# Kernel tuning notes

Hardware: AMD Instinct MI355X
Metric: run time of the kernel (lower is better)

## Reference

```python
import jax, jax.numpy as jnp
import numpy as np
from jax import lax

BN_EPS = 1e-5


def _condconv(x, w, b, fc_w, fc_b):
    """CondConv2D: per-sample expert mixing then 3x3 conv (pad=1, stride=1).
    x: [B, Cin, H, W]; w: [E, Cout, Cin, 3, 3]; b: [Cout]; fc_w: [E, Cin]; fc_b: [E].
    """
    B, Cin, H, W = x.shape
    E, Cout, _, kh, kw = w.shape
    pooled = x.mean(axis=(2, 3))                               # [B, Cin] adaptive_avg_pool2d(1,1)+flatten
    rw = jax.nn.sigmoid(pooled @ fc_w.T + fc_b)                # [B, E] routing weights
    kernels = jnp.einsum('be,eoihw->boihw', rw, w)             # [B, Cout, Cin, 3, 3]
    # Batched per-sample conv via grouped conv: groups = B
    xi = x.reshape(1, B * Cin, H, W)
    ker = kernels.reshape(B * Cout, Cin, kh, kw)
    out = lax.conv_general_dilated(
        xi, ker, window_strides=(1, 1), padding=((1, 1), (1, 1)),
        feature_group_count=B,
        dimension_numbers=('NCHW', 'OIHW', 'NCHW'))
    return out.reshape(B, Cout, H, W) + b[None, :, None, None]


def _bn_relu(x, g, b, m, v):
    # eval-mode BatchNorm2d followed by ReLU
    inv = g * lax.rsqrt(v + BN_EPS)
    return jax.nn.relu(x * inv[None, :, None, None] + (b - m * inv)[None, :, None, None])


def setup_inputs() -> dict:
    key = jax.random.key(0)
    ks = jax.random.split(key, 8)
    B, Cin, Cout, H, W, E = 16, 64, 128, 128, 128, 3
    s1 = 1.0 / np.sqrt(Cin * 9)
    s2 = 1.0 / np.sqrt(Cout * 9)
    return {
        'x': jax.random.normal(ks[0], (B, Cin, H, W), jnp.float32),
        'w1': jax.random.normal(ks[1], (E, Cout, Cin, 3, 3), jnp.float32) * s1,
        'b1': jax.random.normal(ks[2], (Cout,), jnp.float32) * s1,
        'fc1_w': jax.random.normal(ks[3], (E, Cin), jnp.float32) / np.sqrt(Cin),
        'fc1_b': jnp.zeros((E,), jnp.float32),
        'bn1_g': jnp.ones((Cout,), jnp.float32),
        'bn1_b': jnp.zeros((Cout,), jnp.float32),
        'bn1_m': jnp.zeros((Cout,), jnp.float32),
        'bn1_v': jnp.ones((Cout,), jnp.float32),
        'w2': jax.random.normal(ks[4], (E, Cout, Cout, 3, 3), jnp.float32) * s2,
        'b2': jax.random.normal(ks[5], (Cout,), jnp.float32) * s2,
        'fc2_w': jax.random.normal(ks[6], (E, Cout), jnp.float32) / np.sqrt(Cout),
        'fc2_b': jnp.zeros((E,), jnp.float32),
        'bn2_g': jnp.ones((Cout,), jnp.float32),
        'bn2_b': jnp.zeros((Cout,), jnp.float32),
        'bn2_m': jnp.zeros((Cout,), jnp.float32),
        'bn2_v': jnp.ones((Cout,), jnp.float32),
    }


def reference(x, w1, b1, fc1_w, fc1_b, bn1_g, bn1_b, bn1_m, bn1_v,
              w2, b2, fc2_w, fc2_b, bn2_g, bn2_b, bn2_m, bn2_v):
    h = _condconv(x, w1, b1, fc1_w, fc1_b)
    h = _bn_relu(h, bn1_g, bn1_b, bn1_m, bn1_v)
    h = _condconv(h, w2, b2, fc2_w, fc2_b)
    h = _bn_relu(h, bn2_g, bn2_b, bn2_m, bn2_v)
    return h
```

## Files before the change

kernel.cpp:

```cpp
#include <hip/hip_runtime.h>
#include <math.h>

#define BN_EPS 1e-5f

typedef short bf16x8 __attribute__((ext_vector_type(8)));
typedef float f32x4 __attribute__((ext_vector_type(4)));
typedef float f32x16 __attribute__((ext_vector_type(16)));
typedef unsigned short ushort8v __attribute__((ext_vector_type(8)));
typedef unsigned int uint;
typedef unsigned short ushort;

__device__ inline ushort f2bf(float f) {
    uint u = __float_as_uint(f);
    uint r = u + 0x7FFFu + ((u >> 16) & 1u);
    return (ushort)(r >> 16);
}
__device__ inline float bf2f(ushort u) { return __uint_as_float(((uint)u) << 16); }

__global__ void scsh_kernel(const float* b1, const float* g1, const float* bb1,
                            const float* m1, const float* v1,
                            const float* b2, const float* g2, const float* bb2,
                            const float* m2, const float* v2,
                            float* scsh1, float* scsh2) {
    int t = threadIdx.x;
    if (t < 128) {
        float sc = g1[t] * rsqrtf(v1[t] + BN_EPS);
        scsh1[t] = sc;
        scsh1[128 + t] = (b1[t] - m1[t]) * sc + bb1[t];
    } else {
        int c = t - 128;
        float sc = g2[c] * rsqrtf(v2[c] + BN_EPS);
        scsh2[c] = sc;
        scsh2[128 + c] = (b2[c] - m2[c]) * sc + bb2[c];
    }
}

__global__ void xprep_kernel(const float* __restrict__ x, ushort* __restrict__ xT,
                             float* __restrict__ pooled1) {
    __shared__ float t[64][65];
    const int b = blockIdx.y;
    const int p0 = blockIdx.x * 64;
    const int tid = threadIdx.x;
#pragma unroll
    for (int it = 0; it < 16; ++it) {
        const int idx = it * 256 + tid;
        const int ci = idx >> 6, p = idx & 63;
        t[ci][p] = x[((size_t)b * 64 + ci) * 16384 + p0 + p];
    }
    __syncthreads();
    const int h = p0 >> 7;
#pragma unroll
    for (int it = 0; it < 2; ++it) {
        const int p = it * 32 + (tid >> 3);
        const int w = (p0 & 127) + p;
        const int c0 = (tid & 7) * 8;
        const int cc = c0 >> 4;
        ushort8v u;
#pragma unroll
        for (int j = 0; j < 8; ++j) u[j] = f2bf(t[c0 + j][p]);
        *(ushort8v*)&xT[(((size_t)(b * 128 + h) * 4 + cc) * 128 + w) * 16 + (c0 & 15)] = u;
    }
    if (tid < 64) {
        float s = 0.f;
#pragma unroll 8
        for (int p = 0; p < 64; ++p) s += t[tid][p];
        atomicAdd(&pooled1[b * 64 + tid], s);
    }
}

__global__ void pool2h_kernel(const ushort* __restrict__ hT, float* __restrict__ pooled2) {
    const int b = blockIdx.x, slab = blockIdx.y;
    const int tid = threadIdx.x;
    const int cc = tid >> 5, o = (tid >> 4) & 1, wb = tid & 15;
    float a[8] = {0.f, 0.f, 0.f, 0.f, 0.f, 0.f, 0.f, 0.f};
    for (int r = 0; r < 4; ++r) {
        const int h = slab * 4 + r;
        const ushort* base = hT + ((size_t)(b * 128 + h) * 8 + cc) * 2048 + o * 8;
#pragma unroll
        for (int k = 0; k < 8; ++k) {
            const ushort8v u = *(const ushort8v*)(base + (wb + k * 16) * 16);
#pragma unroll
            for (int j = 0; j < 8; ++j) a[j] += bf2f(u[j]);
        }
    }
    __shared__ float sp[16][8][17];
    const int grp0 = cc * 2 + o;
#pragma unroll
    for (int j = 0; j < 8; ++j) sp[grp0][j][wb] = a[j];
    __syncthreads();
    if (tid < 128) {
        const int grp = tid >> 3, j = tid & 7;
        float s = 0.f;
#pragma unroll
        for (int k = 0; k < 16; ++k) s += sp[grp][j][k];
        const int c = (grp >> 1) * 16 + (grp & 1) * 8 + j;
        atomicAdd(&pooled2[b * 128 + c], s);
    }
}

template <int CIN>
__global__ void mix_route_kernel(const float* __restrict__ w, const float* __restrict__ pooled,
                                 const float* __restrict__ fcw, const float* __restrict__ fcb,
                                 ushort* __restrict__ wmix) {
    constexpr int NCC = CIN / 16;
    __shared__ float rwl[48];
    const int tid = threadIdx.x;
    if (tid < 48) {
        const int bb = tid / 3, e = tid % 3;
        float d = 0.f;
        for (int c = 0; c < CIN; ++c) d += pooled[bb * CIN + c] * fcw[e * CIN + c];
        const float s = fcb[e] + d * (1.f / 16384.f);
        rwl[tid] = 1.f / (1.f + expf(-s));
    }
    __syncthreads();
    const int co = blockIdx.x;
    const int sw = (co >> 2) & 1;
    for (int b = 0; b < 16; ++b) {
        const float r0 = rwl[b * 3 + 0], r1 = rwl[b * 3 + 1], r2 = rwl[b * 3 + 2];
        for (int idx = tid; idx < CIN * 9; idx += 256) {
            const int ci = idx & (CIN - 1);
            const int tap = idx / CIN;
            const size_t off = ((size_t)co * CIN + ci) * 9 + tap;
            const float m = r0 * w[off]
                          + r1 * w[off + (size_t)128 * CIN * 9]
                          + r2 * w[off + (size_t)2 * 128 * CIN * 9];
            const int cc = ci >> 4, o = (ci >> 3) & 1, e = ci & 7;
            const size_t dst = (((size_t)(b * NCC + cc)) * 2304
                             + (tap * 128 + co) * 2 + (o ^ sw)) * 8 + e;
            wmix[dst] = f2bf(m);
        }
    }
}

template <int CIN, bool TO_BF16>
__global__ __launch_bounds__(512, 2)
void conv_mfma5_kernel(const ushort* __restrict__ xT, const ushort* __restrict__ wmix,
                       const float* __restrict__ scsh,
                       float* __restrict__ outf, ushort* __restrict__ outh) {
    constexpr int NCC = CIN / 16;
    constexpr int IBUF = 24960;
    constexpr int WOFF = 2 * IBUF;
    constexpr int WBUF = 36864;
    __shared__ __align__(16) char smem[123648];

    const int L = ((blockIdx.x & 7) << 6) | (blockIdx.x >> 3);
    const int b = L >> 5;
    const int rt = L & 31;

    const int tid = threadIdx.x;
    const int lane = tid & 63, wid = tid >> 6;
    const int wm = wid >> 2, wn = wid & 3;
    const int l31 = lane & 31, lhi = lane >> 5;

    f32x16 acc[2][4];
#pragma unroll
    for (int i = 0; i < 2; ++i)
#pragma unroll
        for (int j = 0; j < 4; ++j)
#pragma unroll
            for (int r = 0; r < 16; ++r) acc[i][j][r] = 0.f;

    const ushort* inb = xT + (size_t)b * 128 * NCC * 2048;
    const ushort* wmb = wmix + (size_t)b * NCC * 18432;

    auto stage = [&](int bufi, int cc) {
        const ushort* wsrc = wmb + (size_t)cc * 18432;
        for (int j = wid; j < 60; j += 8) {
            if (j < 24) {
                const int r = j >> 2, i = j & 3;
                const int hg = rt * 4 - 1 + r;
                if ((unsigned)hg < 128u) {
                    const int q = i * 64 + lane;
                    const int cm1 = q >> 1;
                    const int so = (q & 1) ^ (((cm1 + 1) >> 2) & 1);
                    const ushort* src = inb + ((size_t)(hg * NCC + cc)) * 2048 + cm1 * 16 + so * 8;
                    __builtin_amdgcn_global_load_lds(
                        (const __attribute__((address_space(1))) void*)src,
                        (__attribute__((address_space(3))) void*)(smem + bufi * IBUF + (r * 260 + 2 + i * 64) * 16),
                        16, 0, 0);
                }
            } else {
                const int k = j - 24;
                const ushort* src = wsrc + k * 512 + lane * 8;
                __builtin_amdgcn_global_load_lds(
                    (const __attribute__((address_space(1))) void*)src,
                    (__attribute__((address_space(3))) void*)(smem + WOFF + bufi * WBUF + k * 1024),
                    16, 0, 0);
            }
        }
    };

    auto taps = [&](int bufi) {
        const char* ldsI = smem + bufi * IBUF;
        const char* ldsW = smem + WOFF + bufi * WBUF;
#pragma unroll
        for (int tap = 0; tap < 9; ++tap) {
            const int dy = tap / 3, dx = tap - dy * 3;
            bf16x8 af[2];
#pragma unroll
            for (int mf = 0; mf < 2; ++mf) {
                const int co = wm * 64 + mf * 32 + l31;
                const int g = (tap * 128 + co) * 2 + (lhi ^ ((co >> 2) & 1));
                af[mf] = *(const bf16x8*)(ldsW + g * 16);
            }
#pragma unroll
            for (int nf = 0; nf < 4; ++nf) {
                const int col = nf * 32 + l31 + dx;
                const int g = (wn + dy) * 260 + col * 2 + (lhi ^ ((col >> 2) & 1));
                const bf16x8 bv = *(const bf16x8*)(ldsI + g * 16);
#pragma unroll
                for (int mf = 0; mf < 2; ++mf)
                    acc[mf][nf] = __builtin_amdgcn_mfma_f32_32x32x16_bf16(
                        af[mf], bv, acc[mf][nf], 0, 0, 0);
            }
        }
    };

    if (tid < 48) {
        const int bi = tid & 1, idx = tid >> 1;
        const int r = idx >> 2, e = idx & 3;
        const int rem = (e < 2) ? e : 256 + e;
        *(f32x4*)(smem + bi * IBUF + (r * 260 + rem) * 16) = f32x4{0.f, 0.f, 0.f, 0.f};
    }
    if (rt == 0 || rt == 31) {
        const int r = (rt == 0) ? 0 : 5;
        for (int g = tid; g < 520; g += 512) {
            const int bi = (g >= 260) ? 1 : 0, gr = g - bi * 260;
            *(f32x4*)(smem + bi * IBUF + (r * 260 + gr) * 16) = f32x4{0.f, 0.f, 0.f, 0.f};
        }
    }

    stage(0, 0);
    asm volatile("s_waitcnt vmcnt(0)" ::: "memory");
    __syncthreads();

    for (int cc = 0; cc < NCC; ++cc) {
        if (cc + 1 < NCC) stage((cc & 1) ^ 1, cc + 1);
        __builtin_amdgcn_sched_barrier(0);
        taps(cc & 1);
        __syncthreads();
    }

    if constexpr (!TO_BF16) {
#pragma unroll
        for (int mf = 0; mf < 2; ++mf) {
            const int cob = wm * 64 + mf * 32 + 4 * lhi;
            f32x4 sc[4], sh[4];
#pragma unroll
            for (int q = 0; q < 4; ++q) {
                sc[q] = *(const f32x4*)&scsh[cob + 8 * q];
                sh[q] = *(const f32x4*)&scsh[128 + cob + 8 * q];
            }
#pragma unroll
            for (int nf = 0; nf < 4; ++nf) {
                const size_t pbase = (size_t)(rt * 4 + wn) * 128 + nf * 32 + l31;
#pragma unroll
                for (int q = 0; q < 4; ++q)
#pragma unroll
                    for (int s = 0; s < 4; ++s) {
                        float y = fmaf(acc[mf][nf][q * 4 + s], sc[q][s], sh[q][s]);
                        y = y > 0.f ? y : 0.f;
                        outf[((size_t)(b * 128 + cob + 8 * q + s)) * 16384 + pbase] = y;
                    }
            }
        }
    } else {
        ushort* sf = (ushort*)smem;
#pragma unroll
        for (int p = 0; p < 2; ++p) {
            if ((wn >> 1) == p) {
                const int lr = wn & 1;
#pragma unroll
                for (int mf = 0; mf < 2; ++mf)
#pragma unroll
                    for (int q = 0; q < 4; ++q) {
                        const int co4 = wm * 64 + mf * 32 + 8 * q + 4 * lhi;
                        const f32x4 sc = *(const f32x4*)&scsh[co4];
                        const f32x4 sh = *(const f32x4*)&scsh[128 + co4];
#pragma unroll
                        for (int nf = 0; nf < 4; ++nf) {
                            const int px = lr * 128 + nf * 32 + l31;
                            float v[4];
#pragma unroll
                            for (int s = 0; s < 4; ++s) {
                                float y = fmaf(acc[mf][nf][q * 4 + s], sc[s], sh[s]);
                                v[s] = y > 0.f ? y : 0.f;
                            }
                            uint2 pk;
                            pk.x = (uint)f2bf(v[0]) | ((uint)f2bf(v[1]) << 16);
                            pk.y = (uint)f2bf(v[2]) | ((uint)f2bf(v[3]) << 16);
                            *(uint2*)&sf[px * 136 + co4] = pk;
                        }
                    }
            }
            __syncthreads();
#pragma unroll
            for (int it = 0; it < 4; ++it) {
                const int id = it * 512 + tid;
                const int lr = id >> 10, cc = (id >> 7) & 7, w = id & 127;
                const uint4 v0 = *(const uint4*)&sf[(lr * 128 + w) * 136 + cc * 16];
                const uint4 v1 = *(const uint4*)&sf[(lr * 128 + w) * 136 + cc * 16 + 8];
                ushort* dst = outh + (((size_t)(b * 128 + rt * 4 + 2 * p + lr)) * 8 + cc) * 2048 + w * 16;
                *(uint4*)dst = v0;
                *(uint4*)(dst + 8) = v1;
            }
            if (p == 0) __syncthreads();
        }
    }
}

extern "C" void kernel_launch(void* const* d_in, const int* in_sizes, int n_in,
                              void* d_out, int out_size, void* d_ws, size_t ws_size,
                              hipStream_t stream) {
    const float* x     = (const float*)d_in[0];
    const float* w1    = (const float*)d_in[1];
    const float* b1    = (const float*)d_in[2];
    const float* fc1_w = (const float*)d_in[3];
    const float* fc1_b = (const float*)d_in[4];
    const float* bn1g  = (const float*)d_in[5];
    const float* bn1b  = (const float*)d_in[6];
    const float* bn1m  = (const float*)d_in[7];
    const float* bn1v  = (const float*)d_in[8];
    const float* w2    = (const float*)d_in[9];
    const float* b2    = (const float*)d_in[10];
    const float* fc2_w = (const float*)d_in[11];
    const float* fc2_b = (const float*)d_in[12];
    const float* bn2g  = (const float*)d_in[13];
    const float* bn2b  = (const float*)d_in[14];
    const float* bn2m  = (const float*)d_in[15];
    const float* bn2v  = (const float*)d_in[16];

    float* out = (float*)d_out;
    char* ws = (char*)d_ws;

    ushort* hT    = (ushort*)(ws + 0);
    ushort* xT    = (ushort*)(ws + 67108864);
    ushort* wmix1 = (ushort*)(ws + 100663296);
    ushort* wmix2 = (ushort*)(ws + 103022592);
    float*  pool1 = (float*) (ws + 107741184);
    float*  pool2 = (float*) (ws + 107745280);
    float*  scsh1 = (float*) (ws + 107753472);
    float*  scsh2 = (float*) (ws + 107754496);

    hipMemsetAsync(pool1, 0, 4096, stream);
    hipMemsetAsync(pool2, 0, 8192, stream);

    scsh_kernel<<<1, 256, 0, stream>>>(b1, bn1g, bn1b, bn1m, bn1v,
                                       b2, bn2g, bn2b, bn2m, bn2v, scsh1, scsh2);

    xprep_kernel<<<dim3(256, 16), 256, 0, stream>>>(x, xT, pool1);
    mix_route_kernel<64><<<128, 256, 0, stream>>>(w1, pool1, fc1_w, fc1_b, wmix1);
    conv_mfma5_kernel<64, true><<<512, 512, 0, stream>>>(
        xT, wmix1, scsh1, nullptr, hT);

    pool2h_kernel<<<dim3(16, 32), 256, 0, stream>>>(hT, pool2);
    mix_route_kernel<128><<<128, 256, 0, stream>>>(w2, pool2, fc2_w, fc2_b, wmix2);
    conv_mfma5_kernel<128, false><<<512, 512, 0, stream>>>(
        hT, wmix2, scsh2, out, nullptr);
}
```

Before: 213.4 us.

## Shrink conv tile to two rows with single-buffered weights and 256-thread blocks

Restructures the conv kernel so each block covers 2 output rows instead of 4, with 4 waves of 256 threads. Each wave now computes all 128 output channels for 64 pixels instead of 64 channels for 128 pixels, and the grid doubles to 1024 blocks. Weights are single-buffered and staged after each compute step behind an extra barrier, which cuts LDS use to about 70KB so more blocks fit per CU. The trade-off is that weight loads are no longer overlapped with compute and the input halo overhead per output row goes up. The bf16 packing also switches to the hardware v_cvt_pk_bf16_f32 instruction.

New measurement: 198.5 us. 1.07x faster.

```diff
diff --git a/kernel.cpp b/kernel.cpp
--- a/kernel.cpp
+++ b/kernel.cpp
@@ -16,6 +16,11 @@
     return (ushort)(r >> 16);
 }
 __device__ inline float bf2f(ushort u) { return __uint_as_float(((uint)u) << 16); }
+__device__ inline uint cvtpk(float lo, float hi) {
+    uint r;
+    asm("v_cvt_pk_bf16_f32 %0, %1, %2" : "=v"(r) : "v"(lo), "v"(hi));
+    return r;
+}
 
 __global__ void scsh_kernel(const float* b1, const float* g1, const float* bb1,
                             const float* m1, const float* v1,
@@ -133,118 +138,129 @@
 }
 
 template <int CIN, bool TO_BF16>
-__global__ __launch_bounds__(512, 2)
-void conv_mfma5_kernel(const ushort* __restrict__ xT, const ushort* __restrict__ wmix,
+__global__ __launch_bounds__(256, 2)
+void conv_mfma7_kernel(const ushort* __restrict__ xT, const ushort* __restrict__ wmix,
                        const float* __restrict__ scsh,
                        float* __restrict__ outf, ushort* __restrict__ outh) {
     constexpr int NCC = CIN / 16;
-    constexpr int IBUF = 24960;
+    constexpr int IBUF = 16640;
     constexpr int WOFF = 2 * IBUF;
-    constexpr int WBUF = 36864;
-    __shared__ __align__(16) char smem[123648];
-
-    const int L = ((blockIdx.x & 7) << 6) | (blockIdx.x >> 3);
-    const int b = L >> 5;
-    const int rt = L & 31;
+    __shared__ __align__(16) char smem[70144];
+
+    const int L = ((blockIdx.x & 7) << 7) | (blockIdx.x >> 3);
+    const int b = L >> 6;
+    const int rt = L & 63;
 
     const int tid = threadIdx.x;
     const int lane = tid & 63, wid = tid >> 6;
-    const int wm = wid >> 2, wn = wid & 3;
     const int l31 = lane & 31, lhi = lane >> 5;
-
-    f32x16 acc[2][4];
-#pragma unroll
-    for (int i = 0; i < 2; ++i)
-#pragma unroll
-        for (int j = 0; j < 4; ++j)
+    const int wrow = wid >> 1, wcol = (wid & 1) * 64;
+
+    f32x16 acc[4][2];
+#pragma unroll
+    for (int i = 0; i < 4; ++i)
+#pragma unroll
+        for (int j = 0; j < 2; ++j)
 #pragma unroll
             for (int r = 0; r < 16; ++r) acc[i][j][r] = 0.f;
 
     const ushort* inb = xT + (size_t)b * 128 * NCC * 2048;
     const ushort* wmb = wmix + (size_t)b * NCC * 18432;
 
-    auto stage = [&](int bufi, int cc) {
-        const ushort* wsrc = wmb + (size_t)cc * 18432;
-        for (int j = wid; j < 60; j += 8) {
-            if (j < 24) {
-                const int r = j >> 2, i = j & 3;
-                const int hg = rt * 4 - 1 + r;
-                if ((unsigned)hg < 128u) {
-                    const int q = i * 64 + lane;
-                    const int cm1 = q >> 1;
-                    const int so = (q & 1) ^ (((cm1 + 1) >> 2) & 1);
-                    const ushort* src = inb + ((size_t)(hg * NCC + cc)) * 2048 + cm1 * 16 + so * 8;
-                    __builtin_amdgcn_global_load_lds(
-                        (const __attribute__((address_space(1))) void*)src,
-                        (__attribute__((address_space(3))) void*)(smem + bufi * IBUF + (r * 260 + 2 + i * 64) * 16),
-                        16, 0, 0);
-                }
-            } else {
-                const int k = j - 24;
-                const ushort* src = wsrc + k * 512 + lane * 8;
+    const int iq   = wid * 64 + lane;
+    const int icm  = iq >> 1;
+    const int iso  = (iq & 1) ^ (((icm + 1) >> 2) & 1);
+    const int voff_in = icm * 16 + iso * 8;
+    const int hg0  = rt * 2 - 1;
+    const int dsti0 = (2 + iq) * 16;
+    const int wsoff = wid * 512 + lane * 8;
+    const int wdst0 = WOFF + wid * 1024 + lane * 16;
+
+    auto stage_I = [&](int bufi, int cc) {
+        const int ccoff = cc * 2048;
+#pragma unroll
+        for (int u = 0; u < 4; ++u) {
+            const int hg = hg0 + u;
+            if ((unsigned)hg < 128u) {
+                const ushort* src = inb + (size_t)hg * (NCC * 2048) + ccoff + voff_in;
                 __builtin_amdgcn_global_load_lds(
                     (const __attribute__((address_space(1))) void*)src,
-                    (__attribute__((address_space(3))) void*)(smem + WOFF + bufi * WBUF + k * 1024),
+                    (__attribute__((address_space(3))) void*)(smem + bufi * IBUF + u * 4160 + dsti0),
                     16, 0, 0);
             }
+        }
+    };
+    auto stage_W = [&](int cc) {
+        const ushort* wsrc = wmb + (size_t)cc * 18432 + wsoff;
+#pragma unroll
+        for (int u = 0; u < 9; ++u) {
+            __builtin_amdgcn_global_load_lds(
+                (const __attribute__((address_space(1))) void*)(wsrc + u * 2048),
+                (__attribute__((address_space(3))) void*)(smem + wdst0 + u * 4096),
+                16, 0, 0);
         }
     };
 
     auto taps = [&](int bufi) {
         const char* ldsI = smem + bufi * IBUF;
-        const char* ldsW = smem + WOFF + bufi * WBUF;
+        const char* ldsW = smem + WOFF;
 #pragma unroll
         for (int tap = 0; tap < 9; ++tap) {
             const int dy = tap / 3, dx = tap - dy * 3;
-            bf16x8 af[2];
-#pragma unroll
-            for (int mf = 0; mf < 2; ++mf) {
-                const int co = wm * 64 + mf * 32 + l31;
+            bf16x8 af[4];
+#pragma unroll
+            for (int mf = 0; mf < 4; ++mf) {
+                const int co = mf * 32 + l31;
                 const int g = (tap * 128 + co) * 2 + (lhi ^ ((co >> 2) & 1));
                 af[mf] = *(const bf16x8*)(ldsW + g * 16);
             }
 #pragma unroll
-            for (int nf = 0; nf < 4; ++nf) {
-                const int col = nf * 32 + l31 + dx;
-                const int g = (wn + dy) * 260 + col * 2 + (lhi ^ ((col >> 2) & 1));
+            for (int nf = 0; nf < 2; ++nf) {
+                const int colp = wcol + nf * 32 + l31 + dx;
+                const int g = (wrow + dy) * 260 + colp * 2 + (lhi ^ ((colp >> 2) & 1));
                 const bf16x8 bv = *(const bf16x8*)(ldsI + g * 16);
 #pragma unroll
-                for (int mf = 0; mf < 2; ++mf)
+                for (int mf = 0; mf < 4; ++mf)
                     acc[mf][nf] = __builtin_amdgcn_mfma_f32_32x32x16_bf16(
                         af[mf], bv, acc[mf][nf], 0, 0, 0);
             }
         }
     };
 
-    if (tid < 48) {
-        const int bi = tid & 1, idx = tid >> 1;
+    if (tid < 32) {
+        const int bi = tid >> 4, idx = tid & 15;
         const int r = idx >> 2, e = idx & 3;
         const int rem = (e < 2) ? e : 256 + e;
         *(f32x4*)(smem + bi * IBUF + (r * 260 + rem) * 16) = f32x4{0.f, 0.f, 0.f, 0.f};
     }
-    if (rt == 0 || rt == 31) {
-        const int r = (rt == 0) ? 0 : 5;
-        for (int g = tid; g < 520; g += 512) {
+    if (rt == 0 || rt == 63) {
+        const int r = (rt == 0) ? 0 : 3;
+        for (int g = tid; g < 520; g += 256) {
             const int bi = (g >= 260) ? 1 : 0, gr = g - bi * 260;
             *(f32x4*)(smem + bi * IBUF + (r * 260 + gr) * 16) = f32x4{0.f, 0.f, 0.f, 0.f};
         }
     }
 
-    stage(0, 0);
+    stage_W(0);
+    stage_I(0, 0);
     asm volatile("s_waitcnt vmcnt(0)" ::: "memory");
     __syncthreads();
 
     for (int cc = 0; cc < NCC; ++cc) {
-        if (cc + 1 < NCC) stage((cc & 1) ^ 1, cc + 1);
+        if (cc + 1 < NCC) stage_I((cc & 1) ^ 1, cc + 1);
         __builtin_amdgcn_sched_barrier(0);
         taps(cc & 1);
         __syncthreads();
+        if (cc + 1 < NCC) {
+            stage_W(cc + 1);
+            __syncthreads();
+        }
     }
 
     if constexpr (!TO_BF16) {
 #pragma unroll
-        for (int mf = 0; mf < 2; ++mf) {
-            const int cob = wm * 64 + mf * 32 + 4 * lhi;
+        for (int mf = 0; mf < 4; ++mf) {
+            const int cob = mf * 32 + 4 * lhi;
             f32x4 sc[4], sh[4];
 #pragma unroll
             for (int q = 0; q < 4; ++q) {
@@ -252,8 +268,8 @@
                 sh[q] = *(const f32x4*)&scsh[128 + cob + 8 * q];
             }
 #pragma unroll
-            for (int nf = 0; nf < 4; ++nf) {
-                const size_t pbase = (size_t)(rt * 4 + wn) * 128 + nf * 32 + l31;
+            for (int nf = 0; nf < 2; ++nf) {
+                const size_t pbase = (size_t)(rt * 2 + wrow) * 128 + wcol + nf * 32 + l31;
 #pragma unroll
                 for (int q = 0; q < 4; ++q)
 #pragma unroll
@@ -267,44 +283,37 @@
     } else {
         ushort* sf = (ushort*)smem;
 #pragma unroll
-        for (int p = 0; p < 2; ++p) {
-            if ((wn >> 1) == p) {
-                const int lr = wn & 1;
-#pragma unroll
-                for (int mf = 0; mf < 2; ++mf)
-#pragma unroll
-                    for (int q = 0; q < 4; ++q) {
-                        const int co4 = wm * 64 + mf * 32 + 8 * q + 4 * lhi;
-                        const f32x4 sc = *(const f32x4*)&scsh[co4];
-                        const f32x4 sh = *(const f32x4*)&scsh[128 + co4];
-#pragma unroll
-                        for (int nf = 0; nf < 4; ++nf) {
-                            const int px = lr * 128 + nf * 32 + l31;
-                            float v[4];
-#pragma unroll
-                            for (int s = 0; s < 4; ++s) {
-                                float y = fmaf(acc[mf][nf][q * 4 + s], sc[s], sh[s]);
-                                v[s] = y > 0.f ? y : 0.f;
-                            }
-                            uint2 pk;
-                            pk.x = (uint)f2bf(v[0]) | ((uint)f2bf(v[1]) << 16);
-                            pk.y = (uint)f2bf(v[2]) | ((uint)f2bf(v[3]) << 16);
-                            *(uint2*)&sf[px * 136 + co4] = pk;
-                        }
+        for (int mf = 0; mf < 4; ++mf)
+#pragma unroll
+            for (int q = 0; q < 4; ++q) {
+                const int co4 = mf * 32 + 8 * q + 4 * lhi;
+                const f32x4 sc = *(const f32x4*)&scsh[co4];
+                const f32x4 sh = *(const f32x4*)&scsh[128 + co4];
+#pragma unroll
+                for (int nf = 0; nf < 2; ++nf) {
+                    const int px = wrow * 128 + wcol + nf * 32 + l31;
+                    float v[4];
+#pragma unroll
+                    for (int s = 0; s < 4; ++s) {
+                        float y = fmaf(acc[mf][nf][q * 4 + s], sc[s], sh[s]);
+                        v[s] = y > 0.f ? y : 0.f;
                     }
-            }
-            __syncthreads();
-#pragma unroll
-            for (int it = 0; it < 4; ++it) {
-                const int id = it * 512 + tid;
-                const int lr = id >> 10, cc = (id >> 7) & 7, w = id & 127;
-                const uint4 v0 = *(const uint4*)&sf[(lr * 128 + w) * 136 + cc * 16];
-                const uint4 v1 = *(const uint4*)&sf[(lr * 128 + w) * 136 + cc * 16 + 8];
-                ushort* dst = outh + (((size_t)(b * 128 + rt * 4 + 2 * p + lr)) * 8 + cc) * 2048 + w * 16;
-                *(uint4*)dst = v0;
-                *(uint4*)(dst + 8) = v1;
-            }
-            if (p == 0) __syncthreads();
+                    uint2 pk;
+                    pk.x = cvtpk(v[0], v[1]);
+                    pk.y = cvtpk(v[2], v[3]);
+                    *(uint2*)&sf[px * 136 + co4] = pk;
+                }
+            }
+        __syncthreads();
+#pragma unroll
+        for (int it = 0; it < 8; ++it) {
+            const int id = it * 256 + tid;
+            const int lr = id >> 10, cc = (id >> 7) & 7, w = id & 127;
+            const uint4 v0 = *(const uint4*)&sf[(lr * 128 + w) * 136 + cc * 16];
+            const uint4 v1 = *(const uint4*)&sf[(lr * 128 + w) * 136 + cc * 16 + 8];
+            ushort* dst = outh + (((size_t)(b * 128 + rt * 2 + lr)) * 8 + cc) * 2048 + w * 16;
+            *(uint4*)dst = v0;
+            *(uint4*)(dst + 8) = v1;
         }
     }
 }
@@ -350,11 +359,11 @@
 
     xprep_kernel<<<dim3(256, 16), 256, 0, stream>>>(x, xT, pool1);
     mix_route_kernel<64><<<128, 256, 0, stream>>>(w1, pool1, fc1_w, fc1_b, wmix1);
-    conv_mfma5_kernel<64, true><<<512, 512, 0, stream>>>(
+    conv_mfma7_kernel<64, true><<<1024, 256, 0, stream>>>(
         xT, wmix1, scsh1, nullptr, hT);
 
     pool2h_kernel<<<dim3(16, 32), 256, 0, stream>>>(hT, pool2);
     mix_route_kernel<128><<<128, 256, 0, stream>>>(w2, pool2, fc2_w, fc2_b, wmix2);
-    conv_mfma5_kernel<128, false><<<512, 512, 0, stream>>>(
+    conv_mfma7_kernel<128, false><<<1024, 256, 0, stream>>>(
         hT, wmix2, scsh2, out, nullptr);
 }
```

## Unswizzle LDS layouts into octet planes and unroll double-buffered conv staging

Applied to the files above, without the earlier changes.

The mixed-weight and input LDS layouts change from XOR-swizzled interleaved octets to separate planes per 8-channel half. Fragment reads then become constant offsets from precomputed per-lane base pointers, with no per-tap address math. The staging loop is restructured with fixed per-wave load assignments and unrolled by two so buffer pointers are compile-time known, and the explicit vmcnt wait before the first barrier is dropped. The bf16 epilogue packing uses the hardware v_cvt_pk_bf16_f32 instruction. Removing the swizzle risks LDS bank conflicts, and dropping the explicit wait relies on __syncthreads to cover the async LDS loads.

New measurement: 201.6 us. -5.5%, faster.

```diff
diff --git a/kernel.cpp b/kernel.cpp
--- a/kernel.cpp
+++ b/kernel.cpp
@@ -16,6 +16,11 @@
     return (ushort)(r >> 16);
 }
 __device__ inline float bf2f(ushort u) { return __uint_as_float(((uint)u) << 16); }
+__device__ inline uint cvtpk(float lo, float hi) {
+    uint r;
+    asm("v_cvt_pk_bf16_f32 %0, %1, %2" : "=v"(r) : "v"(lo), "v"(hi));
+    return r;
+}
 
 __global__ void scsh_kernel(const float* b1, const float* g1, const float* bb1,
                             const float* m1, const float* v1,
@@ -114,7 +119,6 @@
     }
     __syncthreads();
     const int co = blockIdx.x;
-    const int sw = (co >> 2) & 1;
     for (int b = 0; b < 16; ++b) {
         const float r0 = rwl[b * 3 + 0], r1 = rwl[b * 3 + 1], r2 = rwl[b * 3 + 2];
         for (int idx = tid; idx < CIN * 9; idx += 256) {
@@ -125,8 +129,8 @@
                           + r1 * w[off + (size_t)128 * CIN * 9]
                           + r2 * w[off + (size_t)2 * 128 * CIN * 9];
             const int cc = ci >> 4, o = (ci >> 3) & 1, e = ci & 7;
-            const size_t dst = (((size_t)(b * NCC + cc)) * 2304
-                             + (tap * 128 + co) * 2 + (o ^ sw)) * 8 + e;
+            const size_t dst = ((size_t)(b * NCC + cc) * 2304
+                             + tap * 256 + o * 128 + co) * 8 + e;
             wmix[dst] = f2bf(m);
         }
     }
@@ -134,7 +138,7 @@
 
 template <int CIN, bool TO_BF16>
 __global__ __launch_bounds__(512, 2)
-void conv_mfma5_kernel(const ushort* __restrict__ xT, const ushort* __restrict__ wmix,
+void conv_mfma8_kernel(const ushort* __restrict__ xT, const ushort* __restrict__ wmix,
                        const float* __restrict__ scsh,
                        float* __restrict__ outf, ushort* __restrict__ outh) {
     constexpr int NCC = CIN / 16;
@@ -163,51 +167,62 @@
     const ushort* inb = xT + (size_t)b * 128 * NCC * 2048;
     const ushort* wmb = wmix + (size_t)b * NCC * 18432;
 
-    auto stage = [&](int bufi, int cc) {
-        const ushort* wsrc = wmb + (size_t)cc * 18432;
-        for (int j = wid; j < 60; j += 8) {
-            if (j < 24) {
-                const int r = j >> 2, i = j & 3;
-                const int hg = rt * 4 - 1 + r;
-                if ((unsigned)hg < 128u) {
-                    const int q = i * 64 + lane;
-                    const int cm1 = q >> 1;
-                    const int so = (q & 1) ^ (((cm1 + 1) >> 2) & 1);
-                    const ushort* src = inb + ((size_t)(hg * NCC + cc)) * 2048 + cm1 * 16 + so * 8;
-                    __builtin_amdgcn_global_load_lds(
-                        (const __attribute__((address_space(1))) void*)src,
-                        (__attribute__((address_space(3))) void*)(smem + bufi * IBUF + (r * 260 + 2 + i * 64) * 16),
-                        16, 0, 0);
-                }
-            } else {
-                const int k = j - 24;
-                const ushort* src = wsrc + k * 512 + lane * 8;
+    const int ihalf = wid & 1, ioct = (wid >> 1) & 1, ir0 = wid >> 2;
+    const int iv = (ihalf * 64 + lane) * 16 + ioct * 8;
+    const int idst0 = (ir0 * 260 + ioct * 130 + 1 + ihalf * 64) * 16;
+    const int hg0 = rt * 4 - 1 + ir0;
+    const int wo0 = wid * 2048 + lane * 8;
+    const int wd0 = wid * 4096 + lane * 16;
+    const int weo = 16384 + wid * 512 + lane * 8;
+    const int wed = (32 + wid) * 1024 + lane * 16;
+
+    auto stage = [&](char* dI, char* dW, int cc) {
+        const size_t ccI = (size_t)cc * 2048;
+#pragma unroll
+        for (int u = 0; u < 3; ++u) {
+            const int hg = hg0 + 2 * u;
+            if ((unsigned)hg < 128u) {
+                const ushort* src = inb + (size_t)hg * (NCC * 2048) + ccI + iv;
                 __builtin_amdgcn_global_load_lds(
                     (const __attribute__((address_space(1))) void*)src,
-                    (__attribute__((address_space(3))) void*)(smem + WOFF + bufi * WBUF + k * 1024),
+                    (__attribute__((address_space(3))) void*)(dI + idst0 + u * 8320),
                     16, 0, 0);
             }
         }
+        const ushort* ws = wmb + (size_t)cc * 18432;
+#pragma unroll
+        for (int u = 0; u < 4; ++u) {
+            __builtin_amdgcn_global_load_lds(
+                (const __attribute__((address_space(1))) void*)(ws + wo0 + u * 512),
+                (__attribute__((address_space(3))) void*)(dW + wd0 + u * 1024),
+                16, 0, 0);
+        }
+        if (wid < 4) {
+            __builtin_amdgcn_global_load_lds(
+                (const __attribute__((address_space(1))) void*)(ws + weo),
+                (__attribute__((address_space(3))) void*)(dW + wed),
+                16, 0, 0);
+        }
     };
 
-    auto taps = [&](int bufi) {
-        const char* ldsI = smem + bufi * IBUF;
-        const char* ldsW = smem + WOFF + bufi * WBUF;
+    const int ibase = (wn * 260 + lhi * 130 + l31) * 16;
+    const int wbase = (lhi * 128 + wm * 64 + l31) * 16;
+    const char* pI0 = smem + ibase;
+    const char* pI1 = smem + IBUF + ibase;
+    const char* pW0 = smem + WOFF + wbase;
+    const char* pW1 = smem + WOFF + WBUF + wbase;
+
+    auto taps = [&](const char* ldsI, const char* ldsW) {
 #pragma unroll
         for (int tap = 0; tap < 9; ++tap) {
             const int dy = tap / 3, dx = tap - dy * 3;
             bf16x8 af[2];
 #pragma unroll
-            for (int mf = 0; mf < 2; ++mf) {
-                const int co = wm * 64 + mf * 32 + l31;
-                const int g = (tap * 128 + co) * 2 + (lhi ^ ((co >> 2) & 1));
-                af[mf] = *(const bf16x8*)(ldsW + g * 16);
-            }
+            for (int mf = 0; mf < 2; ++mf)
+                af[mf] = *(const bf16x8*)(ldsW + (tap * 4096 + mf * 512));
 #pragma unroll
             for (int nf = 0; nf < 4; ++nf) {
-                const int col = nf * 32 + l31 + dx;
-                const int g = (wn + dy) * 260 + col * 2 + (lhi ^ ((col >> 2) & 1));
-                const bf16x8 bv = *(const bf16x8*)(ldsI + g * 16);
+                const bf16x8 bv = *(const bf16x8*)(ldsI + (dy * 4160 + nf * 512 + dx * 16));
 #pragma unroll
                 for (int mf = 0; mf < 2; ++mf)
                     acc[mf][nf] = __builtin_amdgcn_mfma_f32_32x32x16_bf16(
@@ -217,27 +232,30 @@
     };
 
     if (tid < 48) {
-        const int bi = tid & 1, idx = tid >> 1;
-        const int r = idx >> 2, e = idx & 3;
-        const int rem = (e < 2) ? e : 256 + e;
-        *(f32x4*)(smem + bi * IBUF + (r * 260 + rem) * 16) = f32x4{0.f, 0.f, 0.f, 0.f};
+        const int bi = tid >= 24, idx = tid - bi * 24;
+        const int r = idx >> 2, j = idx & 3;
+        const int g = r * 260 + (j >> 1) * 130 + (j & 1) * 129;
+        *(f32x4*)(smem + bi * IBUF + g * 16) = f32x4{0.f, 0.f, 0.f, 0.f};
     }
     if (rt == 0 || rt == 31) {
         const int r = (rt == 0) ? 0 : 5;
         for (int g = tid; g < 520; g += 512) {
-            const int bi = (g >= 260) ? 1 : 0, gr = g - bi * 260;
+            const int bi = g >= 260, gr = g - bi * 260;
             *(f32x4*)(smem + bi * IBUF + (r * 260 + gr) * 16) = f32x4{0.f, 0.f, 0.f, 0.f};
         }
     }
 
-    stage(0, 0);
-    asm volatile("s_waitcnt vmcnt(0)" ::: "memory");
+    stage(smem, smem + WOFF, 0);
     __syncthreads();
 
-    for (int cc = 0; cc < NCC; ++cc) {
-        if (cc + 1 < NCC) stage((cc & 1) ^ 1, cc + 1);
+    for (int cc = 0; cc < NCC; cc += 2) {
+        stage(smem + IBUF, smem + WOFF + WBUF, cc + 1);
         __builtin_amdgcn_sched_barrier(0);
-        taps(cc & 1);
+        taps(pI0, pW0);
+        __syncthreads();
+        if (cc + 2 < NCC) stage(smem, smem + WOFF, cc + 2);
+        __builtin_amdgcn_sched_barrier(0);
+        taps(pI1, pW1);
         __syncthreads();
     }
 
@@ -287,8 +305,8 @@
                                 v[s] = y > 0.f ? y : 0.f;
                             }
                             uint2 pk;
-                            pk.x = (uint)f2bf(v[0]) | ((uint)f2bf(v[1]) << 16);
-                            pk.y = (uint)f2bf(v[2]) | ((uint)f2bf(v[3]) << 16);
+                            pk.x = cvtpk(v[0], v[1]);
+                            pk.y = cvtpk(v[2], v[3]);
                             *(uint2*)&sf[px * 136 + co4] = pk;
                         }
                     }
@@ -350,11 +368,11 @@
 
     xprep_kernel<<<dim3(256, 16), 256, 0, stream>>>(x, xT, pool1);
     mix_route_kernel<64><<<128, 256, 0, stream>>>(w1, pool1, fc1_w, fc1_b, wmix1);
-    conv_mfma5_kernel<64, true><<<512, 512, 0, stream>>>(
+    conv_mfma8_kernel<64, true><<<512, 512, 0, stream>>>(
         xT, wmix1, scsh1, nullptr, hT);
 
     pool2h_kernel<<<dim3(16, 32), 256, 0, stream>>>(hT, pool2);
     mix_route_kernel<128><<<128, 256, 0, stream>>>(w2, pool2, fc2_w, fc2_b, wmix2);
-    conv_mfma5_kernel<128, false><<<512, 512, 0, stream>>>(
+    conv_mfma8_kernel<128, false><<<512, 512, 0, stream>>>(
         hT, wmix2, scsh2, out, nullptr);
 }
```
